# Kernel tuning notes

Measured on AMD Instinct MI355X. Metric: run time of the kernel, lower is better.

## Reference

```python
import jax, jax.numpy as jnp
import numpy as np

B, M, IN, H, D = 64, 512, 256, 4, 64
N = B * M
E = N * 16


def setup_inputs() -> dict:
    key = jax.random.key(0)
    ks = jax.random.split(key, 12)
    s = 1.0 / np.sqrt(IN)
    return {
        "query_input": jax.random.normal(ks[0], (N, IN), jnp.float32),
        "source_input": jax.random.normal(ks[1], (N, IN), jnp.float32),
        "edge_weight": jax.random.uniform(ks[2], (E,), jnp.float32),
        "Wq_w": jax.random.normal(ks[3], (IN, H * D), jnp.float32) * s,
        "Wq_b": jax.random.normal(ks[4], (H * D,), jnp.float32) * s,
        "Wk_w": jax.random.normal(ks[5], (IN, H * D), jnp.float32) * s,
        "Wk_b": jax.random.normal(ks[6], (H * D,), jnp.float32) * s,
        "Wv_w": jax.random.normal(ks[7], (IN, H * D), jnp.float32) * s,
        "Wv_b": jax.random.normal(ks[8], (H * D,), jnp.float32) * s,
        "n_nodes": jnp.full((B,), M, jnp.int32),
        "edge_index": jax.random.randint(ks[9], (2, E), 0, N, jnp.int32),
    }


def reference(query_input, source_input, edge_weight, Wq_w, Wq_b, Wk_w, Wk_b, Wv_w, Wv_b, n_nodes, edge_index):
    # projections -> [N, H, D]
    q = (query_input @ Wq_w + Wq_b).reshape(N, H, D)
    k = (source_input @ Wk_w + Wk_b).reshape(N, H, D)
    v = (source_input @ Wv_w + Wv_b).reshape(N, H, D)

    # 'simple' kernel attention. Global L2 normalization (torch.norm over whole tensor).
    qn = q / jnp.linalg.norm(q)
    kn = k / jnp.linalg.norm(k)
    # equal-size graphs: padding + mask reduces exactly to a reshape [B, M, H, D]
    q_pad = qn.reshape(B, M, H, D)
    k_pad = kn.reshape(B, M, H, D)
    v_pad = v.reshape(B, M, H, D)
    kv = jnp.einsum('bmhk,bmhv->bhkv', k_pad, v_pad)          # per-graph K^T V
    v_sum = v_pad.sum(axis=1)                                  # [B, H, D] scatter_add over batch
    k_sum = k_pad.sum(axis=1)                                  # [B, H, D]
    numer = jnp.einsum('bmhk,bhkv->bmhv', q_pad, kv) + v_sum[:, None]
    denom = jnp.einsum('bmhk,bhk->bmh', q_pad, k_sum) + n_nodes.astype(q.dtype)[:, None, None]
    attn = (numer / denom[..., None]).reshape(N, H, D)

    # gcn_conv on value: out[c] = sum_{e: col_e = c} w_e * rsqrt(deg[col_e]*deg[row_e]) * v[row_e]
    row, col = edge_index[0], edge_index[1]
    deg = jax.ops.segment_sum(jnp.ones((E,), jnp.float32), col, num_segments=N)
    val = edge_weight / jnp.sqrt(deg[col] * deg[row])
    val = jnp.nan_to_num(val, nan=0.0, posinf=0.0, neginf=0.0)
    gcn = jax.ops.segment_sum(val[:, None, None] * v[row], col, num_segments=N)

    return (attn + gcn).mean(axis=1)  # mean over heads -> [N, D]
```

## Files before the change

### kernel.cpp

```cpp
#include <hip/hip_runtime.h>
#include <hip/hip_bf16.h>

#define NN 32768
#define BB 64
#define MM 512
#define HH 4
#define DD 64
#define INF 256
#define HD 256
#define EE 524288

typedef unsigned short ushort;
typedef unsigned int uint;
typedef short s16x8 __attribute__((ext_vector_type(8)));
typedef ushort u16x8 __attribute__((ext_vector_type(8)));
typedef float f32x4 __attribute__((ext_vector_type(4)));

__device__ __forceinline__ ushort f2bf(float f) {
    uint u = __float_as_uint(f);
    return (ushort)((u + 0x7fffu + ((u >> 16) & 1u)) >> 16);
}
__device__ __forceinline__ float bf2f(ushort u) {
    return __uint_as_float((uint)u << 16);
}
__device__ __forceinline__ uint pkbf(float x, float y) {
    __hip_bfloat162 h = __float22bfloat162_rn(make_float2(x, y));
    return *(uint*)&h;
}

__global__ __launch_bounds__(256) void prep_kernel(
    const float* __restrict__ Wq, const float* __restrict__ Wk,
    const float* __restrict__ Wv, ushort* __restrict__ WT,
    const int* __restrict__ ei, int* __restrict__ deg)
{
    const int bid = blockIdx.x;
    if (bid < 768) {
        const int id = bid * 256 + threadIdx.x;
        const int mat = id >> 16, rem = id & 65535;
        const int n = rem >> 8, kk = rem & 255;
        const float* W = (mat == 0) ? Wq : (mat == 1) ? Wk : Wv;
        WT[id] = f2bf(W[kk * 256 + n]);
    } else {
        const int e = (bid - 768) * 256 + threadIdx.x;
        atomicAdd(&deg[ei[EE + e]], 1);
    }
}

#define BKP 40
#define BPI 32
__global__ __launch_bounds__(256) void qkv_scan(
    const float* __restrict__ Xq, const float* __restrict__ Xs,
    const ushort* __restrict__ WT,
    const float* __restrict__ bq, const float* __restrict__ bk,
    const float* __restrict__ bv,
    ushort* __restrict__ qo, ushort* __restrict__ ko, ushort* __restrict__ vo,
    float* __restrict__ sumsq,
    const int* __restrict__ deg, int* __restrict__ offsets)
{
    __shared__ ushort Asu[128 * BKP];
    __shared__ ushort Bsu[128 * BPI];
    __shared__ float wred[4];
    __shared__ int part[256];

    const int id = blockIdx.x;
    const int t = threadIdx.x;

    if (id == 1536) {
        const int base = t * 128;
        int s = 0;
        for (int i = 0; i < 128; ++i) s += deg[base + i];
        part[t] = s;
        __syncthreads();
        for (int off = 1; off < 256; off <<= 1) {
            int a = part[t];
            int b2 = (t >= off) ? part[t - off] : 0;
            __syncthreads();
            part[t] = a + b2;
            __syncthreads();
        }
        int run = (t == 0) ? 0 : part[t - 1];
        for (int i = 0; i < 128; ++i) { offsets[base + i] = run; run += deg[base + i]; }
        if (t == 255) offsets[NN] = run;
        return;
    }

    const int vv = (id & 7) * 192 + (id >> 3);
    const int rt = vv / 6, ct = vv % 6;
    const int wsel = ct >> 1;
    const float* A    = (wsel == 0) ? Xq : Xs;
    const ushort* W   = WT + (size_t)wsel * 65536;
    const float* bias = (wsel == 0) ? bq : (wsel == 1) ? bk : bv;
    ushort* C         = (wsel == 0) ? qo : (wsel == 1) ? ko : vo;
    const int row0 = rt * 128;
    const int col0 = (ct & 1) * 128;

    const int l = t & 63, w = t >> 6;
    const int fr = l & 15, q4 = l >> 4;
    const int wr = (w & 1) * 64, wc = (w >> 1) * 64;
    const int sr = t >> 1, sh = (t & 1) * 16;

    f32x4 acc[4][4] = {};

    float4 a0, a1, a2, a3;
    u16x8 b0, b1;
    {
        const float* ap = &A[(size_t)(row0 + sr) * INF + sh];
        a0 = *(const float4*)(ap + 0);
        a1 = *(const float4*)(ap + 4);
        a2 = *(const float4*)(ap + 8);
        a3 = *(const float4*)(ap + 12);
        const ushort* bp = &W[(size_t)(col0 + sr) * INF + sh];
        b0 = *(const u16x8*)(bp + 0);
        b1 = *(const u16x8*)(bp + 8);
    }

    for (int it = 0; it < 8; ++it) {
        __syncthreads();
        {
            u16x8 pa0, pa1;
            pa0[0] = f2bf(a0.x); pa0[1] = f2bf(a0.y); pa0[2] = f2bf(a0.z); pa0[3] = f2bf(a0.w);
            pa0[4] = f2bf(a1.x); pa0[5] = f2bf(a1.y); pa0[6] = f2bf(a1.z); pa0[7] = f2bf(a1.w);
            pa1[0] = f2bf(a2.x); pa1[1] = f2bf(a2.y); pa1[2] = f2bf(a2.z); pa1[3] = f2bf(a2.w);
            pa1[4] = f2bf(a3.x); pa1[5] = f2bf(a3.y); pa1[6] = f2bf(a3.z); pa1[7] = f2bf(a3.w);
            *(u16x8*)&Asu[sr * BKP + sh] = pa0;
            *(u16x8*)&Asu[sr * BKP + sh + 8] = pa1;
            *(u16x8*)&Bsu[sr * BPI + sh] = b0;
            *(u16x8*)&Bsu[sr * BPI + sh + 8] = b1;
        }
        __syncthreads();

        if (it < 7) {
            const int k0 = (it + 1) * 32;
            const float* ap = &A[(size_t)(row0 + sr) * INF + k0 + sh];
            a0 = *(const float4*)(ap + 0);
            a1 = *(const float4*)(ap + 4);
            a2 = *(const float4*)(ap + 8);
            a3 = *(const float4*)(ap + 12);
            const ushort* bp = &W[(size_t)(col0 + sr) * INF + k0 + sh];
            b0 = *(const u16x8*)(bp + 0);
            b1 = *(const u16x8*)(bp + 8);
        }

        const int kg = q4 * 8;
        s16x8 af[4], bf[4];
#pragma unroll
        for (int i = 0; i < 4; ++i)
            af[i] = *(const s16x8*)&Asu[(wr + i * 16 + fr) * BKP + kg];
#pragma unroll
        for (int j = 0; j < 4; ++j)
            bf[j] = *(const s16x8*)&Bsu[(wc + j * 16 + fr) * BPI + kg];
#pragma unroll
        for (int i = 0; i < 4; ++i)
#pragma unroll
            for (int j = 0; j < 4; ++j)
                acc[i][j] = __builtin_amdgcn_mfma_f32_16x16x32_bf16(
                    af[i], bf[j], acc[i][j], 0, 0, 0);
    }

    float loc = 0.f;
#pragma unroll
    for (int j = 0; j < 4; ++j) {
        const int colg = col0 + wc + j * 16 + fr;
        const float bj = bias[colg];
#pragma unroll
        for (int i = 0; i < 4; ++i) {
            const int rowg = row0 + wr + i * 16 + q4 * 4;
#pragma unroll
            for (int m = 0; m < 4; ++m) {
                float cv = acc[i][j][m] + bj;
                loc += cv * cv;
                C[(size_t)(rowg + m) * HD + colg] = f2bf(cv);
            }
        }
    }
    if (wsel < 2) {
#pragma unroll
        for (int off = 32; off > 0; off >>= 1) loc += __shfl_down(loc, off, 64);
        if (l == 0) wred[w] = loc;
        __syncthreads();
        if (t == 0) atomicAdd(&sumsq[wsel], wred[0] + wred[1] + wred[2] + wred[3]);
    }
}

#define KVP 136
__global__ __launch_bounds__(256) void kv_vbar(
    const ushort* __restrict__ k16, const ushort* __restrict__ v16,
    float* __restrict__ kv_p, float* __restrict__ ksum_p, float* __restrict__ vsum_p,
    float* __restrict__ vbar)
{
    __shared__ ushort kT[64 * KVP];
    __shared__ ushort vT[64 * KVP];
    const int bid = blockIdx.x;
    const int t = threadIdx.x;

    if (bid >= 1024) {
        const int idx = (bid - 1024) * 1024 + t * 4;
        const int n = idx >> 6, d0 = idx & 63;
        const ushort* vr = &v16[(size_t)n * HD + d0];
        float4 o;
        float* op = (float*)&o;
#pragma unroll
        for (int j = 0; j < 4; ++j)
            op[j] = 0.25f * (bf2f(vr[j]) + bf2f(vr[64 + j]) +
                             bf2f(vr[128 + j]) + bf2f(vr[192 + j]));
        *(float4*)&vbar[idx] = o;
        return;
    }

    const int h = bid & 3, b = (bid >> 2) & 63, z = bid >> 8;
    const int l = t & 63, w = t >> 6;
    const size_t base = (size_t)b * MM * HD + (size_t)h * DD;
    const int m0 = z * 128;

    {
        const int mat = t >> 7;
        const int u = t & 63;
        const int dhalf = (t >> 6) & 1;
        const int r0 = 2 * u;
        const int d0 = dhalf * 32;
        const ushort* src = mat ? v16 : k16;
        ushort* dst = mat ? vT : kT;
        const ushort* p0 = &src[base + (size_t)(m0 + r0) * HD + d0];
        const ushort* p1 = p0 + HD;
        u16x8 ra[4], rb[4];
#pragma unroll
        for (int i = 0; i < 4; ++i) ra[i] = *(const u16x8*)(p0 + 8 * i);
#pragma unroll
        for (int i = 0; i < 4; ++i) rb[i] = *(const u16x8*)(p1 + 8 * i);
#pragma unroll
        for (int i = 0; i < 4; ++i)
#pragma unroll
            for (int jj = 0; jj < 8; ++jj) {
                const int d = d0 + 8 * i + jj;
                uint pk = (uint)ra[i][jj] | ((uint)rb[i][jj] << 16);
                *(uint*)&dst[d * KVP + r0] = pk;
            }
    }
    __syncthreads();

    const int fr = l & 15, q4 = l >> 4, kg = q4 * 8;
    const int wr2 = (w & 1) * 32, wc2 = (w >> 1) * 32;
    s16x8 ones;
#pragma unroll
    for (int i = 0; i < 8; ++i) ones[i] = (short)0x3F80;

    f32x4 acc[2][2] = {};
    f32x4 aks[2] = {};
    f32x4 avs[2] = {};
#pragma unroll
    for (int s = 0; s < 4; ++s) {
        const int mo = s * 32 + kg;
        s16x8 af[2], bf[2];
        af[0] = *(const s16x8*)&kT[(wr2 + fr) * KVP + mo];
        af[1] = *(const s16x8*)&kT[(wr2 + 16 + fr) * KVP + mo];
        bf[0] = *(const s16x8*)&vT[(wc2 + fr) * KVP + mo];
        bf[1] = *(const s16x8*)&vT[(wc2 + 16 + fr) * KVP + mo];
#pragma unroll
        for (int il = 0; il < 2; ++il)
#pragma unroll
            for (int jl = 0; jl < 2; ++jl)
                acc[il][jl] = __builtin_amdgcn_mfma_f32_16x16x32_bf16(
                    af[il], bf[jl], acc[il][jl], 0, 0, 0);
#pragma unroll
        for (int il = 0; il < 2; ++il)
            aks[il] = __builtin_amdgcn_mfma_f32_16x16x32_bf16(
                af[il], ones, aks[il], 0, 0, 0);
#pragma unroll
        for (int jl = 0; jl < 2; ++jl)
            avs[jl] = __builtin_amdgcn_mfma_f32_16x16x32_bf16(
                ones, bf[jl], avs[jl], 0, 0, 0);
    }

    float* kvb = &kv_p[(((size_t)b * HH + h) * 4 + z) * 4096];
#pragma unroll
    for (int jl = 0; jl < 2; ++jl) {
        const int dv = wc2 + 16 * jl + fr;
#pragma unroll
        for (int il = 0; il < 2; ++il) {
            const int dk = wr2 + 16 * il + q4 * 4;
            *(f32x4*)&kvb[(size_t)dv * 64 + dk] = acc[il][jl];
        }
    }
    float* ksb = &ksum_p[(((size_t)b * HH + h) * 4 + z) * 64];
    float* vsb = &vsum_p[(((size_t)b * HH + h) * 4 + z) * 64];
    if (wc2 == 0 && fr == 0) {
#pragma unroll
        for (int il = 0; il < 2; ++il)
#pragma unroll
            for (int m = 0; m < 4; ++m)
                ksb[wr2 + 16 * il + q4 * 4 + m] = aks[il][m];
    }
    if (wr2 == 0 && l < 16) {
        vsb[wc2 + l]      = avs[0][0];
        vsb[wc2 + 16 + l] = avs[1][0];
    }
}

__global__ __launch_bounds__(256) void red_bucket(
    const float* __restrict__ kv_p, const float* __restrict__ ksum_p,
    const float* __restrict__ vsum_p,
    ushort* __restrict__ kv16, float* __restrict__ ksum_f, float* __restrict__ vsum_f,
    const int* __restrict__ ei, const float* __restrict__ ew,
    const int* __restrict__ deg, const int* __restrict__ offsets,
    int* __restrict__ cursor, int2* __restrict__ pairbuf)
{
    const int bid = blockIdx.x;
    const int t = threadIdx.x;

    if (bid < 1024) {
        const int o4 = bid * 1024 + t * 4;
        const int bh = o4 >> 12, off = o4 & 4095;
        const float* p = &kv_p[(size_t)bh * 16384 + off];
        float4 s0 = *(const float4*)p;
        float4 s1 = *(const float4*)(p + 4096);
        float4 s2 = *(const float4*)(p + 8192);
        float4 s3 = *(const float4*)(p + 12288);
        const float r0 = s0.x + s1.x + s2.x + s3.x;
        const float r1 = s0.y + s1.y + s2.y + s3.y;
        const float r2 = s0.z + s1.z + s2.z + s3.z;
        const float r3 = s0.w + s1.w + s2.w + s3.w;
        uint2 pk = make_uint2(pkbf(r0, r1), pkbf(r2, r3));
        *(uint2*)&kv16[(size_t)bh * 4096 + off] = pk;
    } else if (bid < 1152) {
        const int o = (bid - 1024) * 256 + t;
        const float* src = (o < 16384) ? ksum_p : vsum_p;
        float* dst = (o < 16384) ? ksum_f : vsum_f;
        const int oo = o & 16383;
        const int bh = oo >> 6, d = oo & 63;
        const float* p = &src[(size_t)bh * 256 + d];
        dst[oo] = p[0] + p[64] + p[128] + p[192];
    } else {
        const int e = (bid - 1152) * 256 + t;
        const int row = ei[e], col = ei[EE + e];
        const long long prod = (long long)deg[row] * (long long)deg[col];
        float val = 0.f;
        if (prod > 0) val = ew[e] * __frsqrt_rn((float)prod);
        const int pos = atomicAdd(&cursor[col], 1);
        pairbuf[offsets[col] + pos] = make_int2(row, __float_as_int(val));
    }
}

#define AKP 72
__global__ __launch_bounds__(256) void attn_mfma(
    const ushort* __restrict__ q16, const ushort* __restrict__ kv16,
    const float* __restrict__ ksum_f, const float* __restrict__ vsum_f,
    const float* __restrict__ sumsq,
    const int* __restrict__ n_nodes, float* __restrict__ out)
{
    const int b = blockIdx.y;
    const int m0 = blockIdx.x * 64;
    const int t = threadIdx.x;
    const int l = t & 63, w = t >> 6;
    const int fr = l & 15, q4 = l >> 4;
    const int wn = (w & 1) * 32, wd = (w >> 1) * 32;

    __shared__ ushort kvbf[64 * AKP];
    __shared__ float ksum_l[64], vsum_l[64], denom_l[64];

    const float nn = (float)n_nodes[b];
    const float inv = 1.0f / (sqrtf(sumsq[0]) * sqrtf(sumsq[1]));
    f32x4 acco[2][2] = {};

    for (int h = 0; h < HH; ++h) {
        __syncthreads();
        {
            const int dv = t >> 2, dk0 = (t & 3) * 16;
            const ushort* kvg = &kv16[((size_t)(b * HH + h)) * 4096 + dv * 64 + dk0];
            *(uint4*)&kvbf[dv * AKP + dk0]     = *(const uint4*)kvg;
            *(uint4*)&kvbf[dv * AKP + dk0 + 8] = *(const uint4*)(kvg + 8);
        }
        if (t >= 64 && t < 128)
            ksum_l[t - 64] = ksum_f[((size_t)(b * HH + h)) * 64 + t - 64];
        else if (t >= 128 && t < 192)
            vsum_l[t - 128] = vsum_f[((size_t)(b * HH + h)) * 64 + t - 128];
        __syncthreads();

        if (t < 64) {
            const ushort* qr = &q16[((size_t)(b * MM + m0 + t)) * HD + h * DD];
            float dsum = 0.f;
#pragma unroll
            for (int c = 0; c < 8; ++c) {
                u16x8 qq = *(const u16x8*)(qr + 8 * c);
#pragma unroll
                for (int j2 = 0; j2 < 8; ++j2)
                    dsum += bf2f(qq[j2]) * ksum_l[8 * c + j2];
            }
            denom_l[t] = nn + inv * dsum;
        }
        __syncthreads();

        f32x4 pacc[2][2] = {};
#pragma unroll
        for (int kx = 0; kx < 2; ++kx) {
            const int k0 = kx * 32;
            s16x8 af[2], bf[2];
#pragma unroll
            for (int il = 0; il < 2; ++il)
                af[il] = *(const s16x8*)&q16[
                    ((size_t)(b * MM + m0 + wn + 16 * il + fr)) * HD + h * DD + k0 + q4 * 8];
#pragma unroll
            for (int jl = 0; jl < 2; ++jl)
                bf[jl] = *(const s16x8*)&kvbf[(wd + 16 * jl + fr) * AKP + k0 + q4 * 8];
#pragma unroll
            for (int il = 0; il < 2; ++il)
#pragma unroll
                for (int jl = 0; jl < 2; ++jl)
                    pacc[il][jl] = __builtin_amdgcn_mfma_f32_16x16x32_bf16(
                        af[il], bf[jl], pacc[il][jl], 0, 0, 0);
        }
#pragma unroll
        for (int il = 0; il < 2; ++il)
#pragma unroll
            for (int m = 0; m < 4; ++m) {
                const float rden = 0.25f / denom_l[wn + 16 * il + q4 * 4 + m];
#pragma unroll
                for (int jl = 0; jl < 2; ++jl) {
                    const int d = wd + 16 * jl + fr;
                    acco[il][jl][m] += (inv * pacc[il][jl][m] + vsum_l[d]) * rden;
                }
            }
    }

#pragma unroll
    for (int il = 0; il < 2; ++il)
#pragma unroll
        for (int m = 0; m < 4; ++m) {
            const size_t node = (size_t)b * MM + m0 + wn + 16 * il + q4 * 4 + m;
#pragma unroll
            for (int jl = 0; jl < 2; ++jl)
                out[node * DD + wd + 16 * jl + fr] = acco[il][jl][m];
        }
}

__global__ __launch_bounds__(256) void gcn_gather(
    const int* __restrict__ offsets, const int2* __restrict__ pairbuf,
    const float* __restrict__ vbar, float* __restrict__ out)
{
    const int t = blockIdx.x * 256 + threadIdx.x;
    const int n = t >> 6, d = t & 63;
    const int s = offsets[n], e = offsets[n + 1];
    float acc = 0.f;
    int i = s;
    for (; i + 4 <= e; i += 4) {
        const int2 p0 = pairbuf[i],     p1 = pairbuf[i + 1];
        const int2 p2 = pairbuf[i + 2], p3 = pairbuf[i + 3];
        acc += __int_as_float(p0.y) * vbar[(size_t)p0.x * DD + d];
        acc += __int_as_float(p1.y) * vbar[(size_t)p1.x * DD + d];
        acc += __int_as_float(p2.y) * vbar[(size_t)p2.x * DD + d];
        acc += __int_as_float(p3.y) * vbar[(size_t)p3.x * DD + d];
    }
    for (; i < e; ++i) {
        const int2 p = pairbuf[i];
        acc += __int_as_float(p.y) * vbar[(size_t)p.x * DD + d];
    }
    out[(size_t)n * DD + d] += acc;
}

extern "C" void kernel_launch(void* const* d_in, const int* in_sizes, int n_in,
                              void* d_out, int out_size, void* d_ws, size_t ws_size,
                              hipStream_t stream)
{
    (void)in_sizes; (void)n_in; (void)out_size; (void)ws_size;
    const float* Xq = (const float*)d_in[0];
    const float* Xs = (const float*)d_in[1];
    const float* ew = (const float*)d_in[2];
    const float* Wq = (const float*)d_in[3];
    const float* bq = (const float*)d_in[4];
    const float* Wk = (const float*)d_in[5];
    const float* bk = (const float*)d_in[6];
    const float* Wv = (const float*)d_in[7];
    const float* bv = (const float*)d_in[8];
    const int* n_nodes = (const int*)d_in[9];
    const int* ei = (const int*)d_in[10];
    float* out = (float*)d_out;
    float* ws  = (float*)d_ws;

    const size_t SZ_QKV   = (size_t)NN * HD / 2;
    const size_t OFF_Q    = 0;
    const size_t OFF_K    = SZ_QKV;
    const size_t OFF_V    = SZ_QKV * 2;
    const size_t OFF_SS   = SZ_QKV * 3;
    const size_t OFF_DEG  = OFF_SS + 16;
    const size_t OFF_CUR  = OFF_DEG + NN;
    const size_t OFF_WT   = OFF_CUR + NN;
    const size_t OFF_KV   = OFF_WT + 3 * 65536 / 2;
    const size_t OFF_KSP  = OFF_KV + (size_t)BB * HH * 4 * 4096;
    const size_t OFF_VSP  = OFF_KSP + (size_t)BB * HH * 4 * 64;
    const size_t OFF_KV16 = OFF_VSP + (size_t)BB * HH * 4 * 64;
    const size_t OFF_KSF  = OFF_KV16 + (size_t)BB * HH * 4096 / 2;
    const size_t OFF_VSF  = OFF_KSF + (size_t)BB * HH * 64;
    const size_t OFF_OFFS = OFF_VSF + (size_t)BB * HH * 64;
    const size_t OFF_PAIR = OFF_OFFS + NN + 16;
    const size_t OFF_VBAR = OFF_PAIR + 2 * (size_t)EE;

    ushort* q16   = (ushort*)(ws + OFF_Q);
    ushort* k16   = (ushort*)(ws + OFF_K);
    ushort* v16   = (ushort*)(ws + OFF_V);
    float* sumsq  = ws + OFF_SS;
    int*   deg    = (int*)(ws + OFF_DEG);
    int*   cursor = (int*)(ws + OFF_CUR);
    ushort* WT    = (ushort*)(ws + OFF_WT);
    float* kv_p   = ws + OFF_KV;
    float* ksum_p = ws + OFF_KSP;
    float* vsum_p = ws + OFF_VSP;
    ushort* kv16  = (ushort*)(ws + OFF_KV16);
    float* ksum_f = ws + OFF_KSF;
    float* vsum_f = ws + OFF_VSF;
    int*   offs   = (int*)(ws + OFF_OFFS);
    int2*  pairb  = (int2*)(ws + OFF_PAIR);
    float* vbar   = ws + OFF_VBAR;

    hipMemsetAsync(sumsq, 0, (16 + 2 * NN) * sizeof(float), stream);
    prep_kernel<<<2816, 256, 0, stream>>>(Wq, Wk, Wv, WT, ei, deg);
    qkv_scan<<<1537, 256, 0, stream>>>(
        Xq, Xs, WT, bq, bk, bv, q16, k16, v16, sumsq, deg, offs);
    kv_vbar<<<3072, 256, 0, stream>>>(k16, v16, kv_p, ksum_p, vsum_p, vbar);
    red_bucket<<<3200, 256, 0, stream>>>(
        kv_p, ksum_p, vsum_p, kv16, ksum_f, vsum_f,
        ei, ew, deg, offs, cursor, pairb);
    attn_mfma<<<dim3(MM / 64, BB), 256, 0, stream>>>(
        q16, kv16, ksum_f, vsum_f, sumsq, n_nodes, out);
    gcn_gather<<<(NN * DD) / 256, 256, 0, stream>>>(offs, pairb, vbar, out);
}
```

Baseline: 271.6 us.

## Pre-convert inputs to bf16, async LDS double-buffer in GEMM, vectorize gcn gather

The prep kernel now converts both fp32 input matrices to bf16 in workspace, so the QKV GEMM no longer converts them inline. The GEMM uses global_load_lds async copies into double-buffered shared tiles with one barrier per iteration instead of two. The GCN gather now has each thread handle four features with float4 loads, and the workspace is re-laid out so the bf16 inputs alias the kv buffers. The extra conversion pass adds a full read and write of the inputs, and the unpadded LDS tiles may cause bank conflicts.

```diff
diff --git a/kernel.cpp b/kernel.cpp
--- a/kernel.cpp
+++ b/kernel.cpp
@@ -9,6 +9,7 @@
 #define INF 256
 #define HD 256
 #define EE 524288
+#define XSZ 8388608
 
 typedef unsigned short ushort;
 typedef unsigned int uint;
@@ -28,10 +29,16 @@
     return *(uint*)&h;
 }
 
+#define GLD16(gp, lp) __builtin_amdgcn_global_load_lds( \
+    (const __attribute__((address_space(1))) void*)(gp), \
+    (__attribute__((address_space(3))) void*)(lp), 16, 0, 0)
+
 __global__ __launch_bounds__(256) void prep_kernel(
     const float* __restrict__ Wq, const float* __restrict__ Wk,
     const float* __restrict__ Wv, ushort* __restrict__ WT,
-    const int* __restrict__ ei, int* __restrict__ deg)
+    const int* __restrict__ ei, int* __restrict__ deg,
+    const float* __restrict__ Xq, const float* __restrict__ Xs,
+    ushort* __restrict__ xq16, ushort* __restrict__ xs16)
 {
     const int bid = blockIdx.x;
     if (bid < 768) {
@@ -40,16 +47,26 @@
         const int n = rem >> 8, kk = rem & 255;
         const float* W = (mat == 0) ? Wq : (mat == 1) ? Wk : Wv;
         WT[id] = f2bf(W[kk * 256 + n]);
-    } else {
+    } else if (bid < 2816) {
         const int e = (bid - 768) * 256 + threadIdx.x;
         atomicAdd(&deg[ei[EE + e]], 1);
-    }
-}
-
-#define BKP 40
-#define BPI 32
+    } else {
+        const size_t id = (size_t)(bid - 2816) * 256 + threadIdx.x;
+        const size_t o8 = id * 8;
+        const float* src; ushort* dst; size_t o;
+        if (o8 < XSZ) { src = Xq; dst = xq16; o = o8; }
+        else          { src = Xs; dst = xs16; o = o8 - XSZ; }
+        const float4 f0 = *(const float4*)(src + o);
+        const float4 f1 = *(const float4*)(src + o + 4);
+        u16x8 r;
+        r[0] = f2bf(f0.x); r[1] = f2bf(f0.y); r[2] = f2bf(f0.z); r[3] = f2bf(f0.w);
+        r[4] = f2bf(f1.x); r[5] = f2bf(f1.y); r[6] = f2bf(f1.z); r[7] = f2bf(f1.w);
+        *(u16x8*)(dst + o) = r;
+    }
+}
+
 __global__ __launch_bounds__(256) void qkv_scan(
-    const float* __restrict__ Xq, const float* __restrict__ Xs,
+    const ushort* __restrict__ Xq16, const ushort* __restrict__ Xs16,
     const ushort* __restrict__ WT,
     const float* __restrict__ bq, const float* __restrict__ bk,
     const float* __restrict__ bv,
@@ -57,8 +74,8 @@
     float* __restrict__ sumsq,
     const int* __restrict__ deg, int* __restrict__ offsets)
 {
-    __shared__ ushort Asu[128 * BKP];
-    __shared__ ushort Bsu[128 * BPI];
+    __shared__ ushort As[2][128 * 32];
+    __shared__ ushort Bs[2][128 * 32];
     __shared__ float wred[4];
     __shared__ int part[256];
 
@@ -87,7 +104,7 @@
     const int vv = (id & 7) * 192 + (id >> 3);
     const int rt = vv / 6, ct = vv % 6;
     const int wsel = ct >> 1;
-    const float* A    = (wsel == 0) ? Xq : Xs;
+    const ushort* A16 = (wsel == 0) ? Xq16 : Xs16;
     const ushort* W   = WT + (size_t)wsel * 65536;
     const float* bias = (wsel == 0) ? bq : (wsel == 1) ? bk : bv;
     ushort* C         = (wsel == 0) ? qo : (wsel == 1) ? ko : vo;
@@ -97,64 +114,45 @@
     const int l = t & 63, w = t >> 6;
     const int fr = l & 15, q4 = l >> 4;
     const int wr = (w & 1) * 64, wc = (w >> 1) * 64;
-    const int sr = t >> 1, sh = (t & 1) * 16;
+
+    const int srow = (w << 4) + (l >> 2);
+    const int scol = (l & 3) << 3;
+    const ushort* ga = &A16[(size_t)(row0 + srow) * INF + scol];
+    const ushort* gb = &W  [(size_t)(col0 + srow) * INF + scol];
+    const int lbase = (w << 9);
 
     f32x4 acc[4][4] = {};
 
-    float4 a0, a1, a2, a3;
-    u16x8 b0, b1;
-    {
-        const float* ap = &A[(size_t)(row0 + sr) * INF + sh];
-        a0 = *(const float4*)(ap + 0);
-        a1 = *(const float4*)(ap + 4);
-        a2 = *(const float4*)(ap + 8);
-        a3 = *(const float4*)(ap + 12);
-        const ushort* bp = &W[(size_t)(col0 + sr) * INF + sh];
-        b0 = *(const u16x8*)(bp + 0);
-        b1 = *(const u16x8*)(bp + 8);
-    }
-
+    GLD16(ga,             &As[0][lbase]);
+    GLD16(ga + 64 * INF,  &As[0][2048 + lbase]);
+    GLD16(gb,             &Bs[0][lbase]);
+    GLD16(gb + 64 * INF,  &Bs[0][2048 + lbase]);
+
+    int cur = 0;
     for (int it = 0; it < 8; ++it) {
         __syncthreads();
-        {
-            u16x8 pa0, pa1;
-            pa0[0] = f2bf(a0.x); pa0[1] = f2bf(a0.y); pa0[2] = f2bf(a0.z); pa0[3] = f2bf(a0.w);
-            pa0[4] = f2bf(a1.x); pa0[5] = f2bf(a1.y); pa0[6] = f2bf(a1.z); pa0[7] = f2bf(a1.w);
-            pa1[0] = f2bf(a2.x); pa1[1] = f2bf(a2.y); pa1[2] = f2bf(a2.z); pa1[3] = f2bf(a2.w);
-            pa1[4] = f2bf(a3.x); pa1[5] = f2bf(a3.y); pa1[6] = f2bf(a3.z); pa1[7] = f2bf(a3.w);
-            *(u16x8*)&Asu[sr * BKP + sh] = pa0;
-            *(u16x8*)&Asu[sr * BKP + sh + 8] = pa1;
-            *(u16x8*)&Bsu[sr * BPI + sh] = b0;
-            *(u16x8*)&Bsu[sr * BPI + sh + 8] = b1;
-        }
-        __syncthreads();
-
         if (it < 7) {
             const int k0 = (it + 1) * 32;
-            const float* ap = &A[(size_t)(row0 + sr) * INF + k0 + sh];
-            a0 = *(const float4*)(ap + 0);
-            a1 = *(const float4*)(ap + 4);
-            a2 = *(const float4*)(ap + 8);
-            a3 = *(const float4*)(ap + 12);
-            const ushort* bp = &W[(size_t)(col0 + sr) * INF + k0 + sh];
-            b0 = *(const u16x8*)(bp + 0);
-            b1 = *(const u16x8*)(bp + 8);
-        }
-
+            GLD16(ga + k0,            &As[cur ^ 1][lbase]);
+            GLD16(ga + k0 + 64 * INF, &As[cur ^ 1][2048 + lbase]);
+            GLD16(gb + k0,            &Bs[cur ^ 1][lbase]);
+            GLD16(gb + k0 + 64 * INF, &Bs[cur ^ 1][2048 + lbase]);
+        }
         const int kg = q4 * 8;
-        s16x8 af[4], bf[4];
+        s16x8 af[4], bfr[4];
 #pragma unroll
         for (int i = 0; i < 4; ++i)
-            af[i] = *(const s16x8*)&Asu[(wr + i * 16 + fr) * BKP + kg];
+            af[i] = *(const s16x8*)&As[cur][(wr + i * 16 + fr) * 32 + kg];
 #pragma unroll
         for (int j = 0; j < 4; ++j)
-            bf[j] = *(const s16x8*)&Bsu[(wc + j * 16 + fr) * BPI + kg];
+            bfr[j] = *(const s16x8*)&Bs[cur][(wc + j * 16 + fr) * 32 + kg];
 #pragma unroll
         for (int i = 0; i < 4; ++i)
 #pragma unroll
             for (int j = 0; j < 4; ++j)
                 acc[i][j] = __builtin_amdgcn_mfma_f32_16x16x32_bf16(
-                    af[i], bf[j], acc[i][j], 0, 0, 0);
+                    af[i], bfr[j], acc[i][j], 0, 0, 0);
+        cur ^= 1;
     }
 
     float loc = 0.f;
@@ -437,23 +435,29 @@
     const float* __restrict__ vbar, float* __restrict__ out)
 {
     const int t = blockIdx.x * 256 + threadIdx.x;
-    const int n = t >> 6, d = t & 63;
+    const int n = t >> 4, d4 = (t & 15) << 2;
     const int s = offsets[n], e = offsets[n + 1];
-    float acc = 0.f;
+    float ax = 0.f, ay = 0.f, az = 0.f, aw = 0.f;
     int i = s;
-    for (; i + 4 <= e; i += 4) {
-        const int2 p0 = pairbuf[i],     p1 = pairbuf[i + 1];
-        const int2 p2 = pairbuf[i + 2], p3 = pairbuf[i + 3];
-        acc += __int_as_float(p0.y) * vbar[(size_t)p0.x * DD + d];
-        acc += __int_as_float(p1.y) * vbar[(size_t)p1.x * DD + d];
-        acc += __int_as_float(p2.y) * vbar[(size_t)p2.x * DD + d];
-        acc += __int_as_float(p3.y) * vbar[(size_t)p3.x * DD + d];
-    }
-    for (; i < e; ++i) {
+    for (; i + 2 <= e; i += 2) {
+        const int2 p0 = pairbuf[i], p1 = pairbuf[i + 1];
+        const float w0 = __int_as_float(p0.y), w1 = __int_as_float(p1.y);
+        const float4 v0 = *(const float4*)&vbar[(size_t)p0.x * DD + d4];
+        const float4 v1 = *(const float4*)&vbar[(size_t)p1.x * DD + d4];
+        ax += w0 * v0.x + w1 * v1.x;
+        ay += w0 * v0.y + w1 * v1.y;
+        az += w0 * v0.z + w1 * v1.z;
+        aw += w0 * v0.w + w1 * v1.w;
+    }
+    if (i < e) {
         const int2 p = pairbuf[i];
-        acc += __int_as_float(p.y) * vbar[(size_t)p.x * DD + d];
-    }
-    out[(size_t)n * DD + d] += acc;
+        const float wv = __int_as_float(p.y);
+        const float4 v = *(const float4*)&vbar[(size_t)p.x * DD + d4];
+        ax += wv * v.x; ay += wv * v.y; az += wv * v.z; aw += wv * v.w;
+    }
+    float4 o = *(float4*)&out[(size_t)n * DD + d4];
+    o.x += ax; o.y += ay; o.z += az; o.w += aw;
+    *(float4*)&out[(size_t)n * DD + d4] = o;
 }
 
 extern "C" void kernel_launch(void* const* d_in, const int* in_sizes, int n_in,
@@ -483,14 +487,17 @@
     const size_t OFF_DEG  = OFF_SS + 16;
     const size_t OFF_CUR  = OFF_DEG + NN;
     const size_t OFF_WT   = OFF_CUR + NN;
-    const size_t OFF_KV   = OFF_WT + 3 * 65536 / 2;
+    const size_t OFF_OFFS = OFF_WT + 3 * 65536 / 2;
+    const size_t OFF_UNI  = OFF_OFFS + NN + 16;
+    const size_t OFF_XQ16 = OFF_UNI;
+    const size_t OFF_XS16 = OFF_UNI + XSZ / 2;
+    const size_t OFF_KV   = OFF_UNI;
     const size_t OFF_KSP  = OFF_KV + (size_t)BB * HH * 4 * 4096;
     const size_t OFF_VSP  = OFF_KSP + (size_t)BB * HH * 4 * 64;
     const size_t OFF_KV16 = OFF_VSP + (size_t)BB * HH * 4 * 64;
     const size_t OFF_KSF  = OFF_KV16 + (size_t)BB * HH * 4096 / 2;
     const size_t OFF_VSF  = OFF_KSF + (size_t)BB * HH * 64;
-    const size_t OFF_OFFS = OFF_VSF + (size_t)BB * HH * 64;
-    const size_t OFF_PAIR = OFF_OFFS + NN + 16;
+    const size_t OFF_PAIR = OFF_VSF + (size_t)BB * HH * 64;
     const size_t OFF_VBAR = OFF_PAIR + 2 * (size_t)EE;
 
     ushort* q16   = (ushort*)(ws + OFF_Q);
@@ -500,25 +507,27 @@
     int*   deg    = (int*)(ws + OFF_DEG);
     int*   cursor = (int*)(ws + OFF_CUR);
     ushort* WT    = (ushort*)(ws + OFF_WT);
+    int*   offs   = (int*)(ws + OFF_OFFS);
+    ushort* xq16  = (ushort*)(ws + OFF_XQ16);
+    ushort* xs16  = (ushort*)(ws + OFF_XS16);
     float* kv_p   = ws + OFF_KV;
     float* ksum_p = ws + OFF_KSP;
     float* vsum_p = ws + OFF_VSP;
     ushort* kv16  = (ushort*)(ws + OFF_KV16);
     float* ksum_f = ws + OFF_KSF;
     float* vsum_f = ws + OFF_VSF;
-    int*   offs   = (int*)(ws + OFF_OFFS);
     int2*  pairb  = (int2*)(ws + OFF_PAIR);
     float* vbar   = ws + OFF_VBAR;
 
     hipMemsetAsync(sumsq, 0, (16 + 2 * NN) * sizeof(float), stream);
-    prep_kernel<<<2816, 256, 0, stream>>>(Wq, Wk, Wv, WT, ei, deg);
+    prep_kernel<<<11008, 256, 0, stream>>>(Wq, Wk, Wv, WT, ei, deg, Xq, Xs, xq16, xs16);
     qkv_scan<<<1537, 256, 0, stream>>>(
-        Xq, Xs, WT, bq, bk, bv, q16, k16, v16, sumsq, deg, offs);
+        xq16, xs16, WT, bq, bk, bv, q16, k16, v16, sumsq, deg, offs);
     kv_vbar<<<3072, 256, 0, stream>>>(k16, v16, kv_p, ksum_p, vsum_p, vbar);
     red_bucket<<<3200, 256, 0, stream>>>(
         kv_p, ksum_p, vsum_p, kv16, ksum_f, vsum_f,
         ei, ew, deg, offs, cursor, pairb);
     attn_mfma<<<dim3(MM / 64, BB), 256, 0, stream>>>(
         q16, kv16, ksum_f, vsum_f, sumsq, n_nodes, out);
-    gcn_gather<<<(NN * DD) / 256, 256, 0, stream>>>(offs, pairb, vbar, out);
-}
+    gcn_gather<<<(NN * 16) / 256, 256, 0, stream>>>(offs, pairb, vbar, out);
+}
```

Result: faster. 262.3 us (-3.4%).
